# Kernel optimization log

Hardware: AMD Instinct MI355X
Metric: run time of the kernel (lower is better)

The kernel has to match this reference:

```python
import jax, jax.numpy as jnp
import numpy as np

# Module hyperparameters (from init_kwargs)
M = 2049          # NpointsMesh (odd)
TAU = 3e-6        # Gaussian spreading width
XLIMS = (0.0, 1.0)
MU0 = 1.0
L = abs(XLIMS[1] - XLIMS[0])
TWO_PI = 2.0 * np.pi
B, N = 16, 512


def _grids():
    kGrid = jnp.asarray(np.linspace(-(M // 2), M // 2, M), jnp.float32)
    xGrid = jnp.asarray(TWO_PI * np.linspace(XLIMS[0], XLIMS[1], M + 1)[:-1] / L, jnp.float32)
    return kGrid, xGrid


def setup_inputs() -> dict:
    key = jax.random.key(0)
    kx, = jax.random.split(key, 1)
    x = jax.random.uniform(kx, (B, N), dtype=jnp.float32)  # points inside xLims
    kGrid, _ = _grids()
    multRe0 = (4.0 * np.pi / (kGrid ** 2 + MU0 ** 2))[None, :].astype(jnp.float32)
    multRe1 = (4.0 * np.pi / (kGrid ** 2 + 1.0))[None, :].astype(jnp.float32)
    zeros = jnp.zeros((1, M), jnp.float32)
    return {"x": x, "multRe0": multRe0, "multIm0": zeros,
            "multRe1": multRe1, "multIm1": zeros}


def reference(x, multRe0, multIm0, multRe1, multIm1):
    kGrid, xGrid = _grids()
    # Gaussian spreading: (B, N, M)
    diff = x[..., None] * (TWO_PI / L) - xGrid
    g = jnp.exp(-(diff * diff) / (4.0 * TAU))
    red = jnp.sum(g, axis=1)  # (B, M)
    # NOTE: tf.signal.fftshift/ifftshift default to ALL axes; jnp matches that default.
    fftG = jnp.fft.fftshift(jnp.fft.fft(jax.lax.complex(red, jnp.zeros_like(red)))) * (L / TWO_PI)
    deconv = jnp.sqrt(np.pi / TAU) * jnp.exp((kGrid ** 2) * TAU)  # (M,) real
    rfft = fftG * deconv
    Re, Im = jnp.real(rfft), jnp.imag(rfft)

    def mix(mRe, mIm):
        # Faithful to source (incl. its naming quirk): real = mRe*Re - mRe*Im,
        # imag = mIm*Re + mIm*Im
        return jax.lax.complex(mRe * Re - mRe * Im, mIm * Re + mIm * Im)

    multFFT = jnp.stack([mix(multRe0, multIm0), mix(multRe1, multIm1)], axis=1)  # (B, 2, M)
    multDeconv = multFFT * deconv  # broadcast over (B, 2, M)
    irfft = jnp.real(jnp.fft.ifft(jnp.fft.ifftshift(multDeconv)))  # (B, 2, M)
    # local = irfft[:,None,:,:] * g[:,:,None,:]; fmm = sum over mesh / M  -> einsum
    fmm = jnp.einsum('bnm,bcm->bnc', g, irfft) / M  # (B, N, 2)
    return fmm
```

## Files before the change

### kernel.cpp

```cpp
#include <hip/hip_runtime.h>
#include <math.h>

#define MM 2049
#define BB 16
#define NN 512
#define JH 1025
#define JP 1040
#define SZ 8
#define SCH 257
#define JCH 5
#define Z2 4
#define JB 257
#define TCH 9

static constexpr double D_TWO_PI    = 6.283185307179586476925286766559;
static constexpr double D_STEP      = D_TWO_PI / 2049.0;
static constexpr float  F_TWO_PI    = 6.28318530717958647692f;
static constexpr float  INV_4TAU    = 83333.33333333333f;
static constexpr float  PI_OVER_TAU = 1047197.5511965977f;
static constexpr float  TWO_TAU     = 6.0e-6f;
static constexpr float  INV_2PI     = 0.15915494309189533f;
static constexpr float  INV_M       = 1.0f / 2049.0f;
static constexpr float  WINF        = 8.0f;

__global__ void k_sdft1(const float* __restrict__ x, float2* __restrict__ PSp) {
    __shared__ float lred[SCH];
    __shared__ float lx[NN];
    const int b  = blockIdx.y;
    const int z  = blockIdx.z;
    const int s0 = z * SCH;
    const int s1 = min(s0 + SCH, MM);
    const int cnt = s1 - s0;
    for (int i = threadIdx.x; i < SCH; i += 256) lred[i] = 0.0f;
    for (int i = threadIdx.x; i < NN;  i += 256) lx[i] = x[b * NN + i];
    __syncthreads();
    for (int n = threadIdx.x; n < NN; n += 256) {
        float xv = lx[n];
        float xa = xv * F_TWO_PI;
        float p  = xv * (float)MM;
        int m0 = (int)ceilf(p - WINF);  if (m0 < s0) m0 = s0;
        int m1 = (int)floorf(p + WINF); if (m1 > s1 - 1) m1 = s1 - 1;
        for (int m = m0; m <= m1; ++m) {
            float xg = (float)((double)m * D_STEP);
            float d  = xa - xg;
            atomicAdd(&lred[m - s0], expf(-(d * d) * INV_4TAU));
        }
    }
    __syncthreads();
    const int j = blockIdx.x * 256 + threadIdx.x;
    if (j >= JH) return;
    float ct, st;
    { float ang = (float)((double)j * D_STEP); __sincosf(ang, &st, &ct); }
    float c, s;
    { int r0 = (j * s0) % MM; float ph = (float)((double)r0 * D_STEP); __sincosf(ph, &s, &c); }
    float accc = 0.0f, accs = 0.0f;
    for (int i = 0; i < cnt; ++i) {
        float rv = lred[i];
        accc = fmaf(rv, c, accc);
        accs = fmaf(rv, s, accs);
        float t1 = s * st, t2 = s * ct;
        float cn = fmaf(c, ct, -t1);
        float sn = fmaf(c, st,  t2);
        c = cn; s = sn;
    }
    PSp[((size_t)b * SZ + z) * JP + j] = make_float2(accc, accs);
}

__global__ void k_dft2m(const float2* __restrict__ PSp,
                        const float* __restrict__ mRe0, const float* __restrict__ mIm0,
                        const float* __restrict__ mRe1, const float* __restrict__ mIm1,
                        float* __restrict__ irfp) {
    __shared__ float4 lab[JB];
    const int b   = blockIdx.y;
    const int zj  = blockIdx.z;
    const int jb0 = zj * JB;
    const int jb1 = min(jb0 + JB, JH);
    const int cntj = jb1 - jb0;
    for (int i = threadIdx.x; i < cntj; i += 256) {
        const int j = jb0 + i;
        float cs = 0.0f, sn = 0.0f;
        const float2* base = PSp + (size_t)b * SZ * JP + j;
        #pragma unroll
        for (int z = 0; z < SZ; ++z) {
            float2 ps = base[(size_t)z * JP];
            cs += ps.x; sn += ps.y;
        }
        const int msh = j + 1024;
        const float jf = (float)j;
        const float d2 = PI_OVER_TAU * expf(jf * jf * TWO_TAU);
        const float fac = (j == 0) ? 1.0f : 2.0f;
        const float sc = INV_2PI * d2 * fac;
        float4 v;
        v.x =  sc * mRe1[msh] * cs;
        v.y =  sc * mRe0[msh] * cs;
        v.z = -sc * mIm1[msh] * sn;
        v.w = -sc * mIm0[msh] * sn;
        lab[i] = v;
    }
    __syncthreads();
    const int t = blockIdx.x * 256 + threadIdx.x;
    if (t >= MM) return;
    float ct, st;
    { float ang = (float)((double)t * D_STEP); __sincosf(ang, &st, &ct); }
    float c, s;
    { int r0 = (t * jb0) % MM; float ph = (float)((double)r0 * D_STEP); __sincosf(ph, &s, &c); }
    float acc0 = 0.0f, acc1 = 0.0f;
    for (int i = 0; i < cntj; ++i) {
        float4 v = lab[i];
        acc0 = fmaf(v.x,  c, acc0);
        acc0 = fmaf(v.z, -s, acc0);
        acc1 = fmaf(v.y,  c, acc1);
        acc1 = fmaf(v.w, -s, acc1);
        float t1 = s * st, t2 = s * ct;
        float cn = fmaf(c, ct, -t1);
        float sn2 = fmaf(c, st,  t2);
        c = cn; s = sn2;
    }
    float* o = irfp + ((size_t)(zj * BB + b) * 2) * MM + t;
    o[0]  = acc0 * INV_M;
    o[MM] = acc1 * INV_M;
}

__global__ void k_gather(const float* __restrict__ x, const float* __restrict__ irfp,
                         float* __restrict__ out) {
    const int idx = blockIdx.x * blockDim.x + threadIdx.x;
    if (idx >= BB * NN) return;
    const int b = idx / NN;
    float xv = x[idx];
    float xa = xv * F_TWO_PI;
    float p  = xv * (float)MM;
    int m0 = (int)ceilf(p - WINF);  if (m0 < 0) m0 = 0;
    int m1 = (int)floorf(p + WINF); if (m1 > MM - 1) m1 = MM - 1;
    float acc0 = 0.0f, acc1 = 0.0f;
    for (int m = m0; m <= m1; ++m) {
        float xg = (float)((double)m * D_STEP);
        float d  = xa - xg;
        float g  = expf(-(d * d) * INV_4TAU);
        float p0 = 0.0f, p1 = 0.0f;
        #pragma unroll
        for (int z = 0; z < Z2; ++z) {
            const float* base = irfp + ((size_t)(z * BB + b) * 2) * MM;
            p0 += base[m];
            p1 += base[MM + m];
        }
        acc0 = fmaf(g, p0, acc0);
        acc1 = fmaf(g, p1, acc1);
    }
    out[idx * 2 + 0] = acc0 * INV_M;
    out[idx * 2 + 1] = acc1 * INV_M;
}

extern "C" void kernel_launch(void* const* d_in, const int* in_sizes, int n_in,
                              void* d_out, int out_size, void* d_ws, size_t ws_size,
                              hipStream_t stream) {
    const float* x    = (const float*)d_in[0];
    const float* mRe0 = (const float*)d_in[1];
    const float* mIm0 = (const float*)d_in[2];
    const float* mRe1 = (const float*)d_in[3];
    const float* mIm1 = (const float*)d_in[4];
    float* out = (float*)d_out;

    float2* PSp = (float2*)d_ws;
    float*  irfp = (float*)d_ws + (size_t)2 * BB * SZ * JP;

    k_sdft1 <<<dim3(JCH, BB, SZ), 256, 0, stream>>>(x, PSp);
    k_dft2m <<<dim3(TCH, BB, Z2), 256, 0, stream>>>(PSp, mRe0, mIm0, mRe1, mIm1, irfp);
    k_gather<<<(BB * NN + 255) / 256, 256, 0, stream>>>(x, irfp, out);
}
```

Measured before the change: 96.76 us.

## Exploit DFT conjugate symmetry to halve forward and inverse DFT work

```diff
diff --git a/kernel.cpp b/kernel.cpp
--- a/kernel.cpp
+++ b/kernel.cpp
@@ -7,11 +7,11 @@
 #define JH 1025
 #define JP 1040
 #define SZ 8
-#define SCH 257
+#define PCH 128
 #define JCH 5
 #define Z2 4
-#define JB 257
-#define TCH 9
+#define JB2 257
+#define TCH 5
 
 static constexpr double D_TWO_PI    = 6.283185307179586476925286766559;
 static constexpr double D_STEP      = D_TWO_PI / 2049.0;
@@ -24,27 +24,42 @@
 static constexpr float  WINF        = 8.0f;
 
 __global__ void k_sdft1(const float* __restrict__ x, float2* __restrict__ PSp) {
-    __shared__ float lred[SCH];
-    __shared__ float lx[NN];
+    __shared__ float  LA[PCH];
+    __shared__ float  LB[PCH];
+    __shared__ float2 SD[PCH];
+    __shared__ float  Lz;
     const int b  = blockIdx.y;
     const int z  = blockIdx.z;
-    const int s0 = z * SCH;
-    const int s1 = min(s0 + SCH, MM);
-    const int cnt = s1 - s0;
-    for (int i = threadIdx.x; i < SCH; i += 256) lred[i] = 0.0f;
-    for (int i = threadIdx.x; i < NN;  i += 256) lx[i] = x[b * NN + i];
+    const int a0 = 1 + PCH * z;
+    const int b0 = 2049 - PCH * (z + 1);
+    for (int i = threadIdx.x; i < PCH; i += 256) { LA[i] = 0.0f; LB[i] = 0.0f; }
+    if (threadIdx.x == 0) Lz = 0.0f;
     __syncthreads();
     for (int n = threadIdx.x; n < NN; n += 256) {
-        float xv = lx[n];
+        float xv = x[b * NN + n];
         float xa = xv * F_TWO_PI;
         float p  = xv * (float)MM;
-        int m0 = (int)ceilf(p - WINF);  if (m0 < s0) m0 = s0;
-        int m1 = (int)floorf(p + WINF); if (m1 > s1 - 1) m1 = s1 - 1;
+        int m0 = (int)ceilf(p - WINF);  if (m0 < 0) m0 = 0;
+        int m1 = (int)floorf(p + WINF); if (m1 > MM - 1) m1 = MM - 1;
+        bool hitA = (m1 >= a0) && (m0 <= a0 + PCH - 1);
+        bool hitB = (m1 >= b0) && (m0 <= b0 + PCH - 1);
+        bool hit0 = (z == 0) && (m0 == 0);
+        if (!(hitA || hitB || hit0)) continue;
         for (int m = m0; m <= m1; ++m) {
             float xg = (float)((double)m * D_STEP);
             float d  = xa - xg;
-            atomicAdd(&lred[m - s0], expf(-(d * d) * INV_4TAU));
+            float g  = expf(-(d * d) * INV_4TAU);
+            unsigned ia = (unsigned)(m - a0);
+            unsigned ib = (unsigned)(m - b0);
+            if (ia < PCH) atomicAdd(&LA[ia], g);
+            if (ib < PCH) atomicAdd(&LB[ib], g);
+            if (hit0 && m == 0) atomicAdd(&Lz, g);
         }
+    }
+    __syncthreads();
+    for (int i = threadIdx.x; i < PCH; i += 256) {
+        float ra = LA[i], rb = LB[PCH - 1 - i];
+        SD[i] = make_float2(ra + rb, ra - rb);
     }
     __syncthreads();
     const int j = blockIdx.x * 256 + threadIdx.x;
@@ -52,17 +67,19 @@
     float ct, st;
     { float ang = (float)((double)j * D_STEP); __sincosf(ang, &st, &ct); }
     float c, s;
-    { int r0 = (j * s0) % MM; float ph = (float)((double)r0 * D_STEP); __sincosf(ph, &s, &c); }
+    { int r0 = (j * a0) % MM; float ph = (float)((double)r0 * D_STEP); __sincosf(ph, &s, &c); }
     float accc = 0.0f, accs = 0.0f;
-    for (int i = 0; i < cnt; ++i) {
-        float rv = lred[i];
-        accc = fmaf(rv, c, accc);
-        accs = fmaf(rv, s, accs);
+    #pragma unroll 4
+    for (int i = 0; i < PCH; ++i) {
+        float2 sd = SD[i];
+        accc = fmaf(sd.x, c, accc);
+        accs = fmaf(sd.y, s, accs);
         float t1 = s * st, t2 = s * ct;
         float cn = fmaf(c, ct, -t1);
         float sn = fmaf(c, st,  t2);
         c = cn; s = sn;
     }
+    if (z == 0) accc += Lz;
     PSp[((size_t)b * SZ + z) * JP + j] = make_float2(accc, accs);
 }
 
@@ -70,11 +87,11 @@
                         const float* __restrict__ mRe0, const float* __restrict__ mIm0,
                         const float* __restrict__ mRe1, const float* __restrict__ mIm1,
                         float* __restrict__ irfp) {
-    __shared__ float4 lab[JB];
+    __shared__ float4 lab[JB2];
     const int b   = blockIdx.y;
     const int zj  = blockIdx.z;
-    const int jb0 = zj * JB;
-    const int jb1 = min(jb0 + JB, JH);
+    const int jb0 = zj * JB2;
+    const int jb1 = min(jb0 + JB2, JH);
     const int cntj = jb1 - jb0;
     for (int i = threadIdx.x; i < cntj; i += 256) {
         const int j = jb0 + i;
@@ -99,26 +116,31 @@
     }
     __syncthreads();
     const int t = blockIdx.x * 256 + threadIdx.x;
-    if (t >= MM) return;
+    if (t >= JH) return;
     float ct, st;
     { float ang = (float)((double)t * D_STEP); __sincosf(ang, &st, &ct); }
     float c, s;
     { int r0 = (t * jb0) % MM; float ph = (float)((double)r0 * D_STEP); __sincosf(ph, &s, &c); }
-    float acc0 = 0.0f, acc1 = 0.0f;
+    float E0 = 0.0f, O0 = 0.0f, E1 = 0.0f, O1 = 0.0f;
+    #pragma unroll 4
     for (int i = 0; i < cntj; ++i) {
         float4 v = lab[i];
-        acc0 = fmaf(v.x,  c, acc0);
-        acc0 = fmaf(v.z, -s, acc0);
-        acc1 = fmaf(v.y,  c, acc1);
-        acc1 = fmaf(v.w, -s, acc1);
+        E0 = fmaf(v.x, c, E0);
+        O0 = fmaf(v.z, s, O0);
+        E1 = fmaf(v.y, c, E1);
+        O1 = fmaf(v.w, s, O1);
         float t1 = s * st, t2 = s * ct;
         float cn = fmaf(c, ct, -t1);
         float sn2 = fmaf(c, st,  t2);
         c = cn; s = sn2;
     }
-    float* o = irfp + ((size_t)(zj * BB + b) * 2) * MM + t;
-    o[0]  = acc0 * INV_M;
-    o[MM] = acc1 * INV_M;
+    float* o = irfp + ((size_t)(zj * BB + b) * MM) * 2;
+    o[t * 2 + 0] = (E0 - O0) * INV_M;
+    o[t * 2 + 1] = (E1 - O1) * INV_M;
+    if (t >= 1) {
+        o[(MM - t) * 2 + 0] = (E0 + O0) * INV_M;
+        o[(MM - t) * 2 + 1] = (E1 + O1) * INV_M;
+    }
 }
 
 __global__ void k_gather(const float* __restrict__ x, const float* __restrict__ irfp,
@@ -139,9 +161,10 @@
         float p0 = 0.0f, p1 = 0.0f;
         #pragma unroll
         for (int z = 0; z < Z2; ++z) {
-            const float* base = irfp + ((size_t)(z * BB + b) * 2) * MM;
-            p0 += base[m];
-            p1 += base[MM + m];
+            const float2* base = (const float2*)(irfp + ((size_t)(z * BB + b) * MM) * 2);
+            float2 v = base[m];
+            p0 += v.x;
+            p1 += v.y;
         }
         acc0 = fmaf(g, p0, acc0);
         acc1 = fmaf(g, p1, acc1);
@@ -160,7 +183,7 @@
     const float* mIm1 = (const float*)d_in[4];
     float* out = (float*)d_out;
 
-    float2* PSp = (float2*)d_ws;
+    float2* PSp  = (float2*)d_ws;
     float*  irfp = (float*)d_ws + (size_t)2 * BB * SZ * JP;
 
     k_sdft1 <<<dim3(JCH, BB, SZ), 256, 0, stream>>>(x, PSp);
```

Result: faster. 89.70 us, median of 2 (-7.3%).
